# Performance work log

Measured on AMD Instinct MI355X. Metric: run time of the kernel, lower is better.

Reference implementation:

```python
import jax, jax.numpy as jnp
import numpy as np


def setup_inputs() -> dict:
    key = jax.random.key(0)
    P, B, S = 128, 128, 4096
    k1, k2, k3, k4 = jax.random.split(key, 4)
    # SPD inducing Gram K_ii
    A = jax.random.normal(k1, (P, 2 * P), jnp.float32)
    K_ii = A @ A.T / (2.0 * P) + 1e-2 * jnp.eye(P, dtype=jnp.float32)
    # cross-covariances [B, S, P]
    K_ti = jax.random.normal(k2, (B, S, P), jnp.float32) * 0.1
    # diagonal K_t must dominate the quadratic form so the Schur complement is positive
    Kii_inv = jnp.linalg.inv(K_ii)
    qf = jnp.einsum('bsp,pq,bsq->bs', K_ti, Kii_inv, K_ti)
    K_t = qf + jax.random.uniform(k3, (B, S), jnp.float32) + 0.1
    # learned parameters
    V = jax.random.normal(k4, (P, P), jnp.float32) / jnp.sqrt(P) + jnp.eye(P, dtype=jnp.float32)
    latent_Gscale = jnp.zeros((), jnp.float32)
    dof = 128
    return dict(K_ii=K_ii, K_ti=K_ti, K_t=K_t, V=V, latent_Gscale=latent_Gscale, dof=dof)


def reference(K_ii, K_ti, K_t, V, latent_Gscale, dof):
    P = K_ii.shape[0]
    ti = K_ti.reshape(-1, P)          # [N, P]
    tt = K_t.reshape(-1)              # [N]
    # pos_inv via Cholesky (SPD inverse)
    L = jnp.linalg.cholesky(K_ii)
    Kii_inv = jax.scipy.linalg.cho_solve((L, True), jnp.eye(P, dtype=K_ii.dtype))
    A = ti @ Kii_inv                  # Kti_inv_Kii_flat, [N, P]
    ktt_i = tt - jnp.sum(A * ti, -1)  # Schur complement diag
    # G = V V^T / P * exp(scale)
    G = (V @ V.T) / V.shape[1] * jnp.exp(latent_Gscale)
    Gti = A @ G                       # [N, P]
    gt = jnp.sum(Gti * A, -1) + ktt_i
    # objective: -0.5 * dof * (-(logdet G + logdet Kinv) + tr(Kinv G) - P)
    trace_term = jnp.sum(Kii_inv * G.T)
    logdet_G = jnp.linalg.slogdet(G)[1]
    logdet_Kinv = -2.0 * jnp.sum(jnp.log(jnp.diag(L)))
    obj = -0.5 * dof * (-(logdet_G + logdet_Kinv) + trace_term - P)
    Gii = G
    return (Gii, Gti.reshape(K_ti.shape), gt.reshape(K_t.shape), obj)
```

## Files before the change

kernel.cpp:

```cpp
#include <hip/hip_runtime.h>
#include <cstdint>

typedef __attribute__((ext_vector_type(8))) short short8;
typedef __attribute__((ext_vector_type(4))) float f32x4;

__device__ __forceinline__ unsigned short f2bf(float f) {
    uint32_t u = __builtin_bit_cast(uint32_t, f);
    u += 0x7FFFu + ((u >> 16) & 1u);
    return (unsigned short)(u >> 16);
}

#define SG_OFF   16384
#define SM1_OFF  32768
#define SY_OFF   49152
#define SX_OFF   65536
#define SD_OFF   81920

__global__ __launch_bounds__(256) void k0_G(
    const float* __restrict__ V, const float* __restrict__ gs,
    float* __restrict__ out)
{
    float* sG = out + SG_OFF;
    const float egs = expf(gs[0]) * (1.0f / 128.0f);
    const int ty = threadIdx.x >> 5, tx = threadIdx.x & 31;
    const int r = blockIdx.x * 8 + ty;
    const f32x4* V4 = (const f32x4*)V;
    f32x4 acc = {0.f, 0.f, 0.f, 0.f};
    for (int kq = 0; kq < 32; ++kq) {
        const f32x4 vr = V4[r * 32 + kq];
        #pragma unroll
        for (int e = 0; e < 4; ++e) {
            const f32x4 vc = V4[(tx * 4 + e) * 32 + kq];
            acc[e] += vr[0]*vc[0] + vr[1]*vc[1] + vr[2]*vc[2] + vr[3]*vc[3];
        }
    }
    acc *= egs;
    *(f32x4*)&out[r * 128 + tx * 4] = acc;
    *(f32x4*)&sG[r * 128 + tx * 4] = acc;
}

__global__ __launch_bounds__(512) void k1_factor(
    const float* __restrict__ Kii, float* __restrict__ out)
{
    __shared__ float colA[2][128], colB[2][128], rowX[2][128];
    __shared__ float sDk[128], sDg[128], sRed[4];

    const int tid = threadIdx.x;
    const int ty = tid >> 5, tx = tid & 31;
    const int I0 = ty * 8, J0 = tx * 4;
    const float* sG = out + SG_OFF;
    float* sX = out + SX_OFF;
    float* dbuf = out + SD_OFF;

    f32x4 rA[8], rB[8], rX[8];
    #pragma unroll
    for (int r = 0; r < 8; ++r) {
        rA[r] = *(const f32x4*)&Kii[(size_t)(I0 + r) * 128 + J0];
        rB[r] = *(const f32x4*)&sG[(I0 + r) * 128 + J0];
        f32x4 z = {0.f, 0.f, 0.f, 0.f};
        #pragma unroll
        for (int e = 0; e < 4; ++e) z[e] = (I0 + r == J0 + e) ? 1.0f : 0.0f;
        rX[r] = z;
    }
    if (tx == 0) {
        #pragma unroll
        for (int r = 0; r < 8; ++r) { colA[0][I0 + r] = rA[r][0]; colB[0][I0 + r] = rB[r][0]; }
    }
    if (ty == 0) {
        #pragma unroll
        for (int e = 0; e < 4; ++e) rowX[0][J0 + e] = rX[0][e];
    }
    __syncthreads();

    for (int k = 0; k < 127; ++k) {
        const int b = k & 1;
        const float dK = colA[b][k], dG = colB[b][k];
        const float rdK = 1.0f / dK, rdG = 1.0f / dG;
        if (tid == 0) { sDk[k] = dK; sDg[k] = dG; }

        f32x4 caj = *(const f32x4*)&colA[b][J0];
        f32x4 cbj = *(const f32x4*)&colB[b][J0];
        const f32x4 xj = *(const f32x4*)&rowX[b][J0];
        #pragma unroll
        for (int e = 0; e < 4; ++e)
            if (J0 + e <= k) { caj[e] = 0.0f; cbj[e] = 0.0f; }

        f32x4 ca0 = *(const f32x4*)&colA[b][I0];
        f32x4 ca1 = *(const f32x4*)&colA[b][I0 + 4];
        f32x4 cb0 = *(const f32x4*)&colB[b][I0];
        f32x4 cb1 = *(const f32x4*)&colB[b][I0 + 4];
        #pragma unroll
        for (int r = 0; r < 4; ++r) {
            if (I0 + r <= k)     { ca0[r] = 0.0f; cb0[r] = 0.0f; }
            if (I0 + 4 + r <= k) { ca1[r] = 0.0f; cb1[r] = 0.0f; }
        }

        if (I0 + 7 > k) {
            #pragma unroll
            for (int r = 0; r < 8; ++r) {
                const float am = (r < 4) ? ca0[r & 3] : ca1[r & 3];
                const float bm = (r < 4) ? cb0[r & 3] : cb1[r & 3];
                const float fA = am * rdK;
                const float fB = bm * rdG;
                rA[r] -= fA * caj;
                rB[r] -= fB * cbj;
                rX[r] -= fA * xj;
            }
        }

        const int kn = k + 1, bn = kn & 1;
        if (tx == (kn >> 2)) {
            const int es = kn & 3;
            #pragma unroll
            for (int ee = 0; ee < 4; ++ee) if (ee == es) {
                #pragma unroll
                for (int r = 0; r < 8; ++r) {
                    colA[bn][I0 + r] = rA[r][ee];
                    colB[bn][I0 + r] = rB[r][ee];
                }
            }
        }
        if (ty == (kn >> 3)) {
            const int rs = kn & 7;
            #pragma unroll
            for (int rr = 0; rr < 8; ++rr) if (rr == rs) {
                #pragma unroll
                for (int e = 0; e < 4; ++e) rowX[bn][J0 + e] = rX[rr][e];
            }
        }
        __syncthreads();
    }
    if (tid == 511) { sDk[127] = rA[7][3]; sDg[127] = rB[7][3]; }

    #pragma unroll
    for (int r = 0; r < 8; ++r)
        *(f32x4*)&sX[(I0 + r) * 128 + J0] = rX[r];
    __syncthreads();

    if (tid < 128) {
        dbuf[tid] = sDk[tid];
        float lk = logf(sDk[tid]);
        float lg = logf(sDg[tid]);
        #pragma unroll
        for (int o = 32; o > 0; o >>= 1) { lk += __shfl_xor(lk, o, 64); lg += __shfl_xor(lg, o, 64); }
        if ((tid & 63) == 0) { sRed[(tid >> 6) * 2] = lk; sRed[(tid >> 6) * 2 + 1] = lg; }
    }
    __syncthreads();
    if (tid == 0) {
        dbuf[128] = sRed[0] + sRed[2];
        dbuf[129] = sRed[1] + sRed[3];
    }
}

__global__ __launch_bounds__(256) void k2_M1(float* __restrict__ out)
{
    const float* sX = out + SX_OFF;
    const float* dbuf = out + SD_OFF;
    float* sM1 = out + SM1_OFF;
    __shared__ float srd[128];
    const int tid = threadIdx.x;
    if (tid < 128) srd[tid] = 1.0f / dbuf[tid];
    __syncthreads();
    const int ty = tid >> 5, tx = tid & 31;
    const int a = blockIdx.x * 8 + ty;
    const f32x4* X4 = (const f32x4*)sX;
    f32x4 acc = {0.f, 0.f, 0.f, 0.f};
    for (int k = a; k < 128; ++k) {
        const float xa = sX[k * 128 + a] * srd[k];
        acc += xa * X4[k * 32 + tx];
    }
    *(f32x4*)&sM1[a * 128 + tx * 4] = acc;
}

__global__ __launch_bounds__(256) void k3_Y(float* __restrict__ out, char* __restrict__ wsb)
{
    const float* sG = out + SG_OFF;
    const float* sM1 = out + SM1_OFF;
    float* sY = out + SY_OFF;
    float* dbuf = out + SD_OFF;
    const int tid = threadIdx.x;
    const int ty = tid >> 5, tx = tid & 31;
    const int c = blockIdx.x * 8 + ty;
    const f32x4* M14 = (const f32x4*)sM1;
    f32x4 acc = {0.f, 0.f, 0.f, 0.f};
    for (int m = 0; m < 128; ++m)
        acc += sG[c * 128 + m] * M14[m * 32 + tx];
    *(f32x4*)&sY[c * 128 + tx * 4] = acc;
    const uint32_t lo = (uint32_t)f2bf(acc[0]) | ((uint32_t)f2bf(acc[1]) << 16);
    const uint32_t hi = (uint32_t)f2bf(acc[2]) | ((uint32_t)f2bf(acc[3]) << 16);
    const uint32_t byteoff = (uint32_t)((c * 256 + tx * 8) ^ ((c & 7) << 4));
    *(uint2*)(wsb + byteoff) = make_uint2(lo, hi);
    float t;
    {
        const f32x4* G4 = (const f32x4*)sG;
        const int idx = blockIdx.x * 256 + tid;
        const f32x4 g = G4[idx], mm = M14[idx];
        t = g[0]*mm[0] + g[1]*mm[1] + g[2]*mm[2] + g[3]*mm[3];
    }
    #pragma unroll
    for (int o = 32; o > 0; o >>= 1) t += __shfl_xor(t, o, 64);
    __shared__ float sp[4];
    if ((tid & 63) == 0) sp[tid >> 6] = t;
    __syncthreads();
    if (tid == 0) dbuf[132 + blockIdx.x] = sp[0] + sp[1] + sp[2] + sp[3];
}

__global__ __launch_bounds__(256) void k4_Q(
    float* __restrict__ out, char* __restrict__ wsb, const int* __restrict__ dofp)
{
    const float* sM1 = out + SM1_OFF;
    const float* sY = out + SY_OFF;
    const float* dbuf = out + SD_OFF;
    const int tid = threadIdx.x;
    const int ty = tid >> 5, tx = tid & 31;
    const int c = blockIdx.x * 8 + ty;
    const f32x4* Y4 = (const f32x4*)sY;
    const f32x4* M14 = (const f32x4*)sM1;
    f32x4 acc = -M14[c * 32 + tx];
    for (int m = 0; m < 128; ++m)
        acc += sM1[c * 128 + m] * Y4[m * 32 + tx];
    const uint32_t lo = (uint32_t)f2bf(acc[0]) | ((uint32_t)f2bf(acc[1]) << 16);
    const uint32_t hi = (uint32_t)f2bf(acc[2]) | ((uint32_t)f2bf(acc[3]) << 16);
    const uint32_t byteoff = (uint32_t)((c * 256 + tx * 8) ^ ((c & 7) << 4));
    *(uint2*)(wsb + 32768 + byteoff) = make_uint2(lo, hi);
    if (blockIdx.x == 0 && tid == 0) {
        float trace = 0.0f;
        for (int i = 0; i < 16; ++i) trace += dbuf[132 + i];
        const float ldK = dbuf[128], ldG = dbuf[129];
        const float dof = (float)dofp[0];
        out[67649536] = -0.5f * dof * (-(ldG - ldK) + trace - 128.0f);
    }
}

__global__ __launch_bounds__(256, 2) void main_kernel(
    const float* __restrict__ Kti, const float* __restrict__ Kt,
    const float* __restrict__ ws, float* __restrict__ Gti,
    float* __restrict__ gt)
{
    __shared__ __align__(16) char smem[67584];
    const int tid = threadIdx.x;
    const int lane = tid & 63, wid = tid >> 6;
    const int l15 = lane & 15, l4 = lane >> 4;
    const int brow = blockIdx.x * 128;

    {
        f32x4* s4 = (f32x4*)smem;
        const f32x4* w4 = (const f32x4*)ws;
        for (int i = tid; i < 4096; i += 256) s4[i] = w4[i];
    }
    __syncthreads();

    const int wrow = wid * 32;
    f32x4 accW[2][8] = {};
    f32x4 accZ[2][8] = {};

    const float* tbase = Kti + (size_t)(brow + wrow + l15) * 128;

    for (int kc = 0; kc < 4; ++kc) {
        const int k0 = kc * 32 + l4 * 8;
        const float* p0 = tbase + k0;
        const float* p1 = p0 + 16 * 128;
        const f32x4 f0a = *(const f32x4*)p0;
        const f32x4 f0b = *(const f32x4*)(p0 + 4);
        const f32x4 f1a = *(const f32x4*)p1;
        const f32x4 f1b = *(const f32x4*)(p1 + 4);
        const short8 a0 = { (short)f2bf(f0a[0]), (short)f2bf(f0a[1]), (short)f2bf(f0a[2]), (short)f2bf(f0a[3]),
                            (short)f2bf(f0b[0]), (short)f2bf(f0b[1]), (short)f2bf(f0b[2]), (short)f2bf(f0b[3]) };
        const short8 a1 = { (short)f2bf(f1a[0]), (short)f2bf(f1a[1]), (short)f2bf(f1a[2]), (short)f2bf(f1a[3]),
                            (short)f2bf(f1b[0]), (short)f2bf(f1b[1]), (short)f2bf(f1b[2]), (short)f2bf(f1b[3]) };
        #pragma unroll
        for (int ct = 0; ct < 8; ++ct) {
            const int c = ct * 16 + l15;
            const int byteoff = (c * 256 + k0 * 2) ^ ((c & 7) << 4);
            const short8 bW = *(const short8*)(smem + byteoff);
            const short8 bQ = *(const short8*)(smem + 32768 + byteoff);
            accW[0][ct] = __builtin_amdgcn_mfma_f32_16x16x32_bf16(a0, bW, accW[0][ct], 0, 0, 0);
            accW[1][ct] = __builtin_amdgcn_mfma_f32_16x16x32_bf16(a1, bW, accW[1][ct], 0, 0, 0);
            accZ[0][ct] = __builtin_amdgcn_mfma_f32_16x16x32_bf16(a0, bQ, accZ[0][ct], 0, 0, 0);
            accZ[1][ct] = __builtin_amdgcn_mfma_f32_16x16x32_bf16(a1, bQ, accZ[1][ct], 0, 0, 0);
        }
    }

    #pragma unroll
    for (int rt = 0; rt < 2; ++rt) {
        #pragma unroll
        for (int r = 0; r < 4; ++r) {
            const int row = brow + wrow + rt * 16 + l4 * 4 + r;
            const float* trow = Kti + (size_t)row * 128;
            float p = 0.0f;
            #pragma unroll
            for (int ct = 0; ct < 8; ++ct) p += accZ[rt][ct][r] * trow[ct * 16 + l15];
            p += __shfl_xor(p, 1, 64);
            p += __shfl_xor(p, 2, 64);
            p += __shfl_xor(p, 4, 64);
            p += __shfl_xor(p, 8, 64);
            if (l15 == 0) gt[row] = Kt[row] + p;
        }
    }

    __syncthreads();
    {
        float* sC = (float*)smem;
        #pragma unroll
        for (int rt = 0; rt < 2; ++rt)
            #pragma unroll
            for (int ct = 0; ct < 8; ++ct)
                #pragma unroll
                for (int r = 0; r < 4; ++r)
                    sC[(wrow + rt * 16 + l4 * 4 + r) * 132 + ct * 16 + l15] = accW[rt][ct][r];
    }
    __syncthreads();
    {
        const float* sC = (const float*)smem;
        #pragma unroll
        for (int it = 0; it < 16; ++it) {
            const int lin = it * 256 + tid;
            const int row = lin >> 5, c4 = (lin & 31) * 4;
            const f32x4 v = *(const f32x4*)&sC[row * 132 + c4];
            *(f32x4*)(Gti + (size_t)(brow + row) * 128 + c4) = v;
        }
    }
}

extern "C" void kernel_launch(void* const* d_in, const int* in_sizes, int n_in,
                              void* d_out, int out_size, void* d_ws, size_t ws_size,
                              hipStream_t stream)
{
    const float* Kii = (const float*)d_in[0];
    const float* Kti = (const float*)d_in[1];
    const float* Kt  = (const float*)d_in[2];
    const float* V   = (const float*)d_in[3];
    const float* gs  = (const float*)d_in[4];
    const int*   dof = (const int*)d_in[5];
    float* out = (float*)d_out;
    float* ws  = (float*)d_ws;

    const int N = in_sizes[2];
    const int nblocks = N / 128;

    k0_G<<<16, 256, 0, stream>>>(V, gs, out);
    k1_factor<<<1, 512, 0, stream>>>(Kii, out);
    k2_M1<<<16, 256, 0, stream>>>(out);
    k3_Y<<<16, 256, 0, stream>>>(out, (char*)ws);
    k4_Q<<<16, 256, 0, stream>>>(out, (char*)ws, dof);
    main_kernel<<<nblocks, 256, 0, stream>>>(Kti, Kt, ws,
                                             out + 16384,
                                             out + 67125248);
}
```

Before: 334.4 us.

## Double rows per block, prefetch Kti before LDS fill, store Gti directly

The main kernel now runs 512 threads over 256 rows per block, so each block loads the shared W/Q operand tiles from workspace half as often. All Kti loads for the row tile are issued before the LDS fill, which overlaps global latency with the workspace copy. The LDS-staged coalesced Gti writeback is replaced by direct per-lane scalar stores, removing two barriers and the shared round-trip. The trade-off is narrower, less coalesced 64-byte store segments and higher register pressure, since all A tiles are now held up front.

```diff
diff --git a/kernel.cpp b/kernel.cpp
--- a/kernel.cpp
+++ b/kernel.cpp
@@ -232,52 +232,63 @@
     }
 }
 
-__global__ __launch_bounds__(256, 2) void main_kernel(
+__global__ __launch_bounds__(512) void main_kernel(
     const float* __restrict__ Kti, const float* __restrict__ Kt,
     const float* __restrict__ ws, float* __restrict__ Gti,
     float* __restrict__ gt)
 {
-    __shared__ __align__(16) char smem[67584];
+    __shared__ __align__(16) char smem[65536];
     const int tid = threadIdx.x;
     const int lane = tid & 63, wid = tid >> 6;
     const int l15 = lane & 15, l4 = lane >> 4;
-    const int brow = blockIdx.x * 128;
+    const int brow = blockIdx.x * 256;
+    const int wrow = wid * 32;
+
+    const float* tbase = Kti + (size_t)(brow + wrow + l15) * 128;
+
+    f32x4 t[4][4];
+    #pragma unroll
+    for (int kc = 0; kc < 4; ++kc) {
+        const float* p0 = tbase + kc * 32 + l4 * 8;
+        const float* p1 = p0 + 16 * 128;
+        t[kc][0] = *(const f32x4*)p0;
+        t[kc][1] = *(const f32x4*)(p0 + 4);
+        t[kc][2] = *(const f32x4*)p1;
+        t[kc][3] = *(const f32x4*)(p1 + 4);
+    }
 
     {
         f32x4* s4 = (f32x4*)smem;
         const f32x4* w4 = (const f32x4*)ws;
-        for (int i = tid; i < 4096; i += 256) s4[i] = w4[i];
-    }
-    __syncthreads();
-
-    const int wrow = wid * 32;
+        #pragma unroll
+        for (int i = 0; i < 8; ++i) s4[tid + i * 512] = w4[tid + i * 512];
+    }
+
+    short8 a[4][2];
+    #pragma unroll
+    for (int kc = 0; kc < 4; ++kc) {
+        a[kc][0] = { (short)f2bf(t[kc][0][0]), (short)f2bf(t[kc][0][1]), (short)f2bf(t[kc][0][2]), (short)f2bf(t[kc][0][3]),
+                     (short)f2bf(t[kc][1][0]), (short)f2bf(t[kc][1][1]), (short)f2bf(t[kc][1][2]), (short)f2bf(t[kc][1][3]) };
+        a[kc][1] = { (short)f2bf(t[kc][2][0]), (short)f2bf(t[kc][2][1]), (short)f2bf(t[kc][2][2]), (short)f2bf(t[kc][2][3]),
+                     (short)f2bf(t[kc][3][0]), (short)f2bf(t[kc][3][1]), (short)f2bf(t[kc][3][2]), (short)f2bf(t[kc][3][3]) };
+    }
+    __syncthreads();
+
     f32x4 accW[2][8] = {};
     f32x4 accZ[2][8] = {};
-
-    const float* tbase = Kti + (size_t)(brow + wrow + l15) * 128;
-
+    #pragma unroll
     for (int kc = 0; kc < 4; ++kc) {
         const int k0 = kc * 32 + l4 * 8;
-        const float* p0 = tbase + k0;
-        const float* p1 = p0 + 16 * 128;
-        const f32x4 f0a = *(const f32x4*)p0;
-        const f32x4 f0b = *(const f32x4*)(p0 + 4);
-        const f32x4 f1a = *(const f32x4*)p1;
-        const f32x4 f1b = *(const f32x4*)(p1 + 4);
-        const short8 a0 = { (short)f2bf(f0a[0]), (short)f2bf(f0a[1]), (short)f2bf(f0a[2]), (short)f2bf(f0a[3]),
-                            (short)f2bf(f0b[0]), (short)f2bf(f0b[1]), (short)f2bf(f0b[2]), (short)f2bf(f0b[3]) };
-        const short8 a1 = { (short)f2bf(f1a[0]), (short)f2bf(f1a[1]), (short)f2bf(f1a[2]), (short)f2bf(f1a[3]),
-                            (short)f2bf(f1b[0]), (short)f2bf(f1b[1]), (short)f2bf(f1b[2]), (short)f2bf(f1b[3]) };
         #pragma unroll
         for (int ct = 0; ct < 8; ++ct) {
             const int c = ct * 16 + l15;
             const int byteoff = (c * 256 + k0 * 2) ^ ((c & 7) << 4);
             const short8 bW = *(const short8*)(smem + byteoff);
             const short8 bQ = *(const short8*)(smem + 32768 + byteoff);
-            accW[0][ct] = __builtin_amdgcn_mfma_f32_16x16x32_bf16(a0, bW, accW[0][ct], 0, 0, 0);
-            accW[1][ct] = __builtin_amdgcn_mfma_f32_16x16x32_bf16(a1, bW, accW[1][ct], 0, 0, 0);
-            accZ[0][ct] = __builtin_amdgcn_mfma_f32_16x16x32_bf16(a0, bQ, accZ[0][ct], 0, 0, 0);
-            accZ[1][ct] = __builtin_amdgcn_mfma_f32_16x16x32_bf16(a1, bQ, accZ[1][ct], 0, 0, 0);
+            accW[0][ct] = __builtin_amdgcn_mfma_f32_16x16x32_bf16(a[kc][0], bW, accW[0][ct], 0, 0, 0);
+            accW[1][ct] = __builtin_amdgcn_mfma_f32_16x16x32_bf16(a[kc][1], bW, accW[1][ct], 0, 0, 0);
+            accZ[0][ct] = __builtin_amdgcn_mfma_f32_16x16x32_bf16(a[kc][0], bQ, accZ[0][ct], 0, 0, 0);
+            accZ[1][ct] = __builtin_amdgcn_mfma_f32_16x16x32_bf16(a[kc][1], bQ, accZ[1][ct], 0, 0, 0);
         }
     }
 
@@ -298,26 +309,14 @@
         }
     }
 
-    __syncthreads();
-    {
-        float* sC = (float*)smem;
-        #pragma unroll
-        for (int rt = 0; rt < 2; ++rt)
+    #pragma unroll
+    for (int rt = 0; rt < 2; ++rt) {
+        #pragma unroll
+        for (int r = 0; r < 4; ++r) {
+            float* grow = Gti + (size_t)(brow + wrow + rt * 16 + l4 * 4 + r) * 128 + l15;
             #pragma unroll
             for (int ct = 0; ct < 8; ++ct)
-                #pragma unroll
-                for (int r = 0; r < 4; ++r)
-                    sC[(wrow + rt * 16 + l4 * 4 + r) * 132 + ct * 16 + l15] = accW[rt][ct][r];
-    }
-    __syncthreads();
-    {
-        const float* sC = (const float*)smem;
-        #pragma unroll
-        for (int it = 0; it < 16; ++it) {
-            const int lin = it * 256 + tid;
-            const int row = lin >> 5, c4 = (lin & 31) * 4;
-            const f32x4 v = *(const f32x4*)&sC[row * 132 + c4];
-            *(f32x4*)(Gti + (size_t)(brow + row) * 128 + c4) = v;
+                grow[ct * 16] = accW[rt][ct][r];
         }
     }
 }
@@ -336,14 +335,14 @@
     float* ws  = (float*)d_ws;
 
     const int N = in_sizes[2];
-    const int nblocks = N / 128;
+    const int nblocks = N / 256;
 
     k0_G<<<16, 256, 0, stream>>>(V, gs, out);
     k1_factor<<<1, 512, 0, stream>>>(Kii, out);
     k2_M1<<<16, 256, 0, stream>>>(out);
     k3_Y<<<16, 256, 0, stream>>>(out, (char*)ws);
     k4_Q<<<16, 256, 0, stream>>>(out, (char*)ws, dof);
-    main_kernel<<<nblocks, 256, 0, stream>>>(Kti, Kt, ws,
+    main_kernel<<<nblocks, 512, 0, stream>>>(Kti, Kt, ws,
                                              out + 16384,
                                              out + 67125248);
 }
```

After: 305.5 us. 8.6% less time.
